# Optimization experiments

Hardware: AMD Instinct MI355X
Metric: run time of the kernel (lower is better)

The kernel has to match this reference:

```python
import jax, jax.numpy as jnp
import numpy as np

B, L, D = 2, 2048, 768
HID = 32           # saliency gate hidden dim
WINDOWS = (8, 32)  # sorted window sizes
CLAMP_MIN, CLAMP_MAX = 0.05, 0.95
SCALE = 1.0 / np.sqrt(D)  # memory_dim == d_model


def setup_inputs() -> dict:
    key = jax.random.key(0)
    ks = jax.random.split(key, 16)
    s = 0.02
    return {
        "hidden_states": jax.random.normal(ks[0], (B, L, D), jnp.float32),
        "saliency_scores": jax.random.uniform(ks[1], (B, L), jnp.float32),
        # SaliencyGate MLP: Linear(1->HID), SiLU, Linear(HID->D)
        "gw1": jax.random.normal(ks[2], (HID, 1), jnp.float32) * s,
        "gb1": jnp.zeros((HID,), jnp.float32),
        "gw2": jax.random.normal(ks[3], (D, HID), jnp.float32) * s,
        "gb2": jnp.zeros((D,), jnp.float32),
        # SelectiveMemory projections
        "wq": jax.random.normal(ks[4], (D, D), jnp.float32) * s,
        "bq": jnp.zeros((D,), jnp.float32),
        "wk": jax.random.normal(ks[5], (D, D), jnp.float32) * s,
        "bk": jnp.zeros((D,), jnp.float32),
        "wv": jax.random.normal(ks[6], (D, D), jnp.float32) * s,
        "bv": jnp.zeros((D,), jnp.float32),
        "wo": jax.random.normal(ks[7], (D, D), jnp.float32) * s,
        "bo": jnp.zeros((D,), jnp.float32),
    }


def _forward(hidden_states, saliency_scores, gw1, gb1, gw2, gb2,
             wq, bq, wk, bk, wv, bv, wo, bo):
    # ---- SaliencyGate: scalar score -> MLP -> sigmoid gate -> clamp ----
    s = saliency_scores[..., None]                          # (b, l, 1)
    h1 = jax.nn.silu(s @ gw1.T + gb1)                       # (b, l, HID)
    gates = jax.nn.sigmoid(h1 @ gw2.T + gb2)                # (b, l, D)
    gates = jnp.clip(gates, CLAMP_MIN, CLAMP_MAX)
    h = hidden_states * gates

    # ---- SelectiveMemory: multi-window local attention ----
    q = h @ wq.T + bq                                       # (b, l, D)
    k = h @ wk.T + bk
    v = h @ wv.T + bv
    # Torch pads hidden_states with zeros before k/v projection; linear of a
    # zero row equals the bias, so padded key/value rows are exactly bk / bv.
    contexts = []
    for w in WINDOWS:
        kp = jnp.concatenate(
            [jnp.broadcast_to(bk, (B, w - 1, D)), k], axis=1)  # (b, l+w-1, D)
        vp = jnp.concatenate(
            [jnp.broadcast_to(bv, (B, w - 1, D)), v], axis=1)
        idx = jnp.arange(L)[:, None] + jnp.arange(w)[None, :]  # (l, w)
        kw = kp[:, idx]                                        # (b, l, w, D)
        vw = vp[:, idx]
        scores = jnp.einsum('bld,blwd->blw', q, kw) * SCALE
        attn = jax.nn.softmax(scores, axis=-1)
        contexts.append(jnp.einsum('blw,blwd->bld', attn, vw))
    merged = (contexts[0] + contexts[1]) * 0.5 if len(contexts) > 1 else contexts[0]
    return h + merged @ wo.T + bo


def reference(hidden_states, saliency_scores, gw1, gb1, gw2, gb2,
              wq, bq, wk, bk, wv, bv, wo, bo):
    return _forward(hidden_states, saliency_scores, gw1, gb1, gw2, gb2,
                    wq, bq, wk, bk, wv, bv, wo, bo)
```

## Files before the change

### kernel.cpp

```cpp
#include <hip/hip_runtime.h>
#include <hip/hip_bf16.h>
#include <stdint.h>

#define Bb 2
#define Ll 2048
#define Dd 768
#define HID 32
#define BL (Bb*Ll)
#define KPAD 32
#define KROWS (KPAD+Ll+16)

typedef __hip_bfloat16 bf16;
typedef __attribute__((ext_vector_type(8))) short short8;
typedef __attribute__((ext_vector_type(4))) short short4s;
typedef __attribute__((ext_vector_type(4))) float floatx4;

__device__ __forceinline__ float b2f(short u) {
    union { float f; unsigned i; } x; x.i = ((unsigned)(unsigned short)u) << 16; return x.f;
}
__device__ __forceinline__ bf16 f2b(float x) { return __float2bfloat16(x); }
__device__ __forceinline__ short f2bs(float x) {
    bf16 t = __float2bfloat16(x);
    union { bf16 h; short s; } u; u.h = t; return u.s;
}

typedef __attribute__((address_space(1))) const unsigned int guint;
typedef __attribute__((address_space(3))) unsigned int luint;
__device__ __forceinline__ void gload16(const bf16* g, bf16* l) {
    __builtin_amdgcn_global_load_lds((guint*)g, (luint*)l, 16, 0, 0);
}

#define CONV_VB 2304
#define KP_VB   (Bb*48)
#define VT_VB   ((Bb*Dd*48)/256)
#define PREP_VB (CONV_VB+KP_VB+VT_VB)
#define GATE_VB (BL/8)
__global__ __launch_bounds__(256) void prep_gate_kernel(
        const float* __restrict__ wq, const float* __restrict__ wk,
        const float* __restrict__ wv, const float* __restrict__ wo,
        const float* __restrict__ bk, const float* __restrict__ bv,
        const float* __restrict__ hidden, const float* __restrict__ sal,
        const float* __restrict__ gw1, const float* __restrict__ gb1,
        const float* __restrict__ gw2, const float* __restrict__ gb2,
        bf16* __restrict__ wout, bf16* __restrict__ kp, bf16* __restrict__ vT,
        bf16* __restrict__ h_b) {
    __shared__ bf16 g2t[32 * 770];
    __shared__ float h1s[8][HID];
    int bx = blockIdx.x, tid = threadIdx.x;
    if (bx < CONV_VB) {
        int idx = bx * 256 + tid;
        const int per = Dd * Dd / 4;
        int w = idx / per, r = idx % per;
        const float* src = (w == 0) ? wq : (w == 1) ? wk : (w == 2) ? wv : wo;
        float4 v = reinterpret_cast<const float4*>(src)[r];
        bf16* o = wout + (size_t)w * Dd * Dd + (size_t)r * 4;
        o[0] = f2b(v.x); o[1] = f2b(v.y); o[2] = f2b(v.z); o[3] = f2b(v.w);
    } else if (bx < CONV_VB + KP_VB) {
        int pb = bx - CONV_VB;
        int b = pb / 48, c = pb % 48;
        int row = (c < 32) ? c : (KPAD + Ll + (c - 32));
        size_t base = ((size_t)b * KROWS + row) * Dd;
        for (int i = tid; i < Dd; i += 256)
            kp[base + i] = (c < 32) ? f2b(bk[i]) : f2b(0.f);
    } else if (bx < PREP_VB) {
        int o = (bx - CONV_VB - KP_VB) * 256 + tid;
        int b = o / (Dd * 48); int rem = o - b * Dd * 48;
        int n = rem / 48, c = rem % 48;
        int col = (c < 32) ? c : (KPAD + Ll + (c - 32));
        vT[((size_t)b * Dd + n) * KROWS + col] = (c < 32) ? f2b(bv[n]) : f2b(0.f);
    } else {
        int row0 = (bx - PREP_VB) * 8;
#pragma unroll
        for (int k2 = 0; k2 < 24; ++k2) {
            int o4 = tid + k2 * 256;
            float4 v = reinterpret_cast<const float4*>(gw2)[o4];
            int d = o4 >> 3, j = (o4 & 7) * 4;
            g2t[(j + 0) * 770 + d] = f2b(v.x);
            g2t[(j + 1) * 770 + d] = f2b(v.y);
            g2t[(j + 2) * 770 + d] = f2b(v.z);
            g2t[(j + 3) * 770 + d] = f2b(v.w);
        }
        {
            int rr = tid >> 5, j = tid & 31;
            float s = sal[row0 + rr];
            float x = s * gw1[j] + gb1[j];
            h1s[rr][j] = x / (1.f + __expf(-x));
        }
        __syncthreads();
#pragma unroll
        for (int dl = 0; dl < 3; ++dl) {
            int d = tid + dl * 256;
            float base = gb2[d];
            float acc[8];
#pragma unroll
            for (int rr = 0; rr < 8; ++rr) acc[rr] = base;
#pragma unroll
            for (int j = 0; j < HID; ++j) {
                float wj = b2f(*(const short*)&g2t[j * 770 + d]);
#pragma unroll
                for (int rr = 0; rr < 8; ++rr) acc[rr] += h1s[rr][j] * wj;
            }
#pragma unroll
            for (int rr = 0; rr < 8; ++rr) {
                float g = 1.f / (1.f + __expf(-acc[rr]));
                g = fminf(fmaxf(g, 0.05f), 0.95f);
                size_t off = (size_t)(row0 + rr) * Dd + d;
                h_b[off] = f2b(hidden[off] * g);
            }
        }
    }
}

template<int NF, int BK>
__device__ __forceinline__ void gemm_core(const bf16* __restrict__ Ag, const bf16* __restrict__ Wg,
                                          int m0, int n0, bf16* As, bf16* Bs,
                                          floatx4 (&acc)[4][NF]) {
    const int tid  = threadIdx.x;
    const int wave = tid >> 6, lane = tid & 63;
    const int lrow = lane & 15, koff = (lane >> 4) * 8;
    const int wm = (wave >> 1) * 64, wn = (wave & 1) * (NF * 16);
    const int RS = BK * 2;
    const char* Asb = (const char*)As;
    const char* Bsb = (const char*)Bs;

    for (int k0 = 0; k0 < Dd; k0 += BK) {
#pragma unroll
        for (int c = 0; c < BK / 16; ++c) {
            int p = tid * 16 + c * 4096;
            int r = p / RS;
            int o = (p % RS) ^ ((r & 7) << 4);
            gload16(Ag + (size_t)(m0 + r) * Dd + k0 + (o >> 1),
                    As + (wave * 1024 + c * 4096) / 2);
        }
#pragma unroll
        for (int c = 0; c < NF * BK / 64; ++c) {
            int p = tid * 16 + c * 4096;
            int r = p / RS;
            int o = (p % RS) ^ ((r & 7) << 4);
            gload16(Wg + (size_t)(n0 + r) * Dd + k0 + (o >> 1),
                    Bs + (wave * 1024 + c * 4096) / 2);
        }
        __syncthreads();
#pragma unroll
        for (int kk = 0; kk < BK; kk += 32) {
            short8 a[4], b[NF];
#pragma unroll
            for (int i = 0; i < 4; ++i) {
                int row = wm + i * 16 + lrow;
                int byt = row * RS + (((kk + koff) * 2) ^ ((row & 7) << 4));
                a[i] = *reinterpret_cast<const short8*>(Asb + byt);
            }
#pragma unroll
            for (int j = 0; j < NF; ++j) {
                int row = wn + j * 16 + lrow;
                int byt = row * RS + (((kk + koff) * 2) ^ ((row & 7) << 4));
                b[j] = *reinterpret_cast<const short8*>(Bsb + byt);
            }
#pragma unroll
            for (int i = 0; i < 4; ++i)
#pragma unroll
                for (int j = 0; j < NF; ++j)
                    acc[i][j] = __builtin_amdgcn_mfma_f32_16x16x32_bf16(a[i], b[j], acc[i][j], 0, 0, 0);
        }
        __syncthreads();
    }
}

__global__ __launch_bounds__(256, 2) void gemm_qkv(
        const bf16* __restrict__ A, const bf16* __restrict__ W3,
        const float* __restrict__ bq, const float* __restrict__ bk, const float* __restrict__ bv,
        bf16* __restrict__ qo, bf16* __restrict__ kp, bf16* __restrict__ vT) {
    __shared__ bf16 As[128 * 128];
    __shared__ bf16 Bs[128 * 128];
    int bid = blockIdx.x;
    int xcd = bid & 7, idx = bid >> 3;
    int mtile = (xcd >> 1) * 8 + (idx & 7);
    int ntile = (xcd & 1) * 9 + (idx >> 3);
    int tgt = ntile / 6;
    int n0 = (ntile % 6) * 128;
    int m0 = mtile * 128;
    const bf16* W = W3 + (size_t)tgt * Dd * Dd;
    const float* bias = (tgt == 0) ? bq : (tgt == 1) ? bk : bv;

    floatx4 acc[4][4] = {};
    gemm_core<4, 128>(A, W, m0, n0, As, Bs, acc);

    int wave = threadIdx.x >> 6, lane = threadIdx.x & 63;
    int wm = (wave >> 1) * 64, wn = (wave & 1) * 64;
    int crow = (lane >> 4) * 4, ccol = lane & 15;
#pragma unroll
    for (int i = 0; i < 4; ++i)
#pragma unroll
        for (int j = 0; j < 4; ++j) {
            int n = n0 + wn + j * 16 + ccol;
            float bb = bias[n];
            int m = m0 + wm + i * 16 + crow;
            int b_ = m >> 11, l = m & 2047;
            if (tgt == 2) {
                short4s pk;
#pragma unroll
                for (int rr = 0; rr < 4; ++rr) pk[rr] = f2bs(acc[i][j][rr] + bb);
                *reinterpret_cast<short4s*>(vT + ((size_t)b_ * Dd + n) * KROWS + KPAD + l) = pk;
            } else {
#pragma unroll
                for (int rr = 0; rr < 4; ++rr) {
                    size_t orow = (tgt == 0) ? (size_t)(m + rr)
                                             : ((size_t)b_ * KROWS + KPAD + l + rr);
                    bf16* outp = (tgt == 0) ? qo : kp;
                    outp[orow * Dd + n] = f2b(acc[i][j][rr] + bb);
                }
            }
        }
}

__global__ __launch_bounds__(256, 2) void gemm_out(
        const bf16* __restrict__ A, const bf16* __restrict__ W,
        const float* __restrict__ bias, const bf16* __restrict__ addend,
        float* __restrict__ out) {
    __shared__ bf16 As[128 * 64];
    __shared__ bf16 Bs[64 * 64];
    int bid = blockIdx.x;
    int xcd = bid & 7, idx = bid >> 3;
    int mtile = (xcd >> 1) * 8 + (idx & 7);
    int ntile = (xcd & 1) * 6 + (idx >> 3);
    int n0 = ntile * 64, m0 = mtile * 128;

    floatx4 acc[4][2] = {};
    gemm_core<2, 64>(A, W, m0, n0, As, Bs, acc);

    int wave = threadIdx.x >> 6, lane = threadIdx.x & 63;
    int wm = (wave >> 1) * 64, wn = (wave & 1) * 32;
    int crow = (lane >> 4) * 4, ccol = lane & 15;
#pragma unroll
    for (int i = 0; i < 4; ++i)
#pragma unroll
        for (int j = 0; j < 2; ++j) {
            int n = n0 + wn + j * 16 + ccol;
            float bb = bias[n];
#pragma unroll
            for (int rr = 0; rr < 4; ++rr) {
                int m = m0 + wm + i * 16 + crow + rr;
                size_t o = (size_t)m * Dd + n;
                out[o] = acc[i][j][rr] + bb + b2f(*(const short*)(addend + o));
            }
        }
}

__global__ __launch_bounds__(64) void attn_kernel(
        const bf16* __restrict__ q, const bf16* __restrict__ kp, const bf16* __restrict__ vT,
        bf16* __restrict__ merged) {
    __shared__ bf16 wlds[16 * 64];
    const int lane = threadIdx.x;
    const int bid = blockIdx.x;
    const int g = (bid & 7) * 32 + (bid >> 3);
    const int b = g >> 7, L0 = (g & 127) * 16;
    const int lrow = lane & 15, koff = (lane >> 4) * 8;
    const int crow = (lane >> 4) * 4, ccol = lane & 15;
    const float scale = 0.03608439182435161f;

    const bf16* qbase = q  + ((size_t)(b * Ll + L0 + lrow)) * Dd + koff;
    const bf16* kbase = kp + ((size_t)b * KROWS + L0 + lrow) * Dd + koff;
    floatx4 s[4] = {};
    for (int ks = 0; ks < 24; ++ks) {
        short8 a = *reinterpret_cast<const short8*>(qbase + ks * 32);
#pragma unroll
        for (int f = 0; f < 4; ++f) {
            short8 bb = *reinterpret_cast<const short8*>(kbase + (size_t)f * 16 * Dd + ks * 32);
            s[f] = __builtin_amdgcn_mfma_f32_16x16x32_bf16(a, bb, s[f], 0, 0, 0);
        }
    }
#pragma unroll
    for (int rr = 0; rr < 4; ++rr) {
        int r = crow + rr;
        float z[4], e[4];
#pragma unroll
        for (int f = 0; f < 4; ++f) {
            int j = f * 16 + ccol;
            bool valid = (j >= r + 1) && (j <= r + 32);
            z[f] = valid ? s[f][rr] * scale : -3.0e38f;
        }
        float m = fmaxf(fmaxf(z[0], z[1]), fmaxf(z[2], z[3]));
#pragma unroll
        for (int off = 1; off < 16; off <<= 1) m = fmaxf(m, __shfl_xor(m, off));
        float S32 = 0.f, S8 = 0.f;
#pragma unroll
        for (int f = 0; f < 4; ++f) {
            e[f] = __expf(z[f] - m);
            S32 += e[f];
            int j = f * 16 + ccol;
            S8 += ((j >= r + 25) && (j <= r + 32)) ? e[f] : 0.f;
        }
#pragma unroll
        for (int off = 1; off < 16; off <<= 1) {
            S32 += __shfl_xor(S32, off);
            S8  += __shfl_xor(S8, off);
        }
        float i32 = 0.5f / S32, i8 = 0.5f / S8;
#pragma unroll
        for (int f = 0; f < 4; ++f) {
            int j = f * 16 + ccol;
            float wgt = e[f] * i32 + (((j >= r + 25) && (j <= r + 32)) ? e[f] * i8 : 0.f);
            int byt = ((r * 64 + j) * 2) ^ ((r & 7) << 4);
            *reinterpret_cast<bf16*>(reinterpret_cast<char*>(wlds) + byt) = f2b(wgt);
        }
    }
    __syncthreads();

    short8 wa[2];
#pragma unroll
    for (int ks = 0; ks < 2; ++ks) {
        int byt = ((lrow * 64 + ks * 32 + koff) * 2) ^ ((lrow & 7) << 4);
        wa[ks] = *reinterpret_cast<const short8*>(reinterpret_cast<const char*>(wlds) + byt);
    }
    const bf16* vbase = vT + (size_t)b * Dd * KROWS + L0;
    bf16* obase = merged + ((size_t)(b * Ll + L0 + ccol)) * Dd;
    for (int c = 0; c < 6; ++c) {
#pragma unroll
        for (int fn = 0; fn < 8; ++fn) {
            int nr = c * 128 + fn * 16;
            floatx4 acc = {};
#pragma unroll
            for (int ks = 0; ks < 2; ++ks) {
                short8 bb = *reinterpret_cast<const short8*>(vbase + (size_t)(nr + lrow) * KROWS + ks * 32 + koff);
                acc = __builtin_amdgcn_mfma_f32_16x16x32_bf16(bb, wa[ks], acc, 0, 0, 0);
            }
            short4s pk;
#pragma unroll
            for (int rr = 0; rr < 4; ++rr) pk[rr] = f2bs(acc[rr]);
            *reinterpret_cast<short4s*>(obase + nr + crow) = pk;
        }
    }
}

extern "C" void kernel_launch(void* const* d_in, const int* in_sizes, int n_in,
                              void* d_out, int out_size, void* d_ws, size_t ws_size,
                              hipStream_t stream) {
    const float* hidden = (const float*)d_in[0];
    const float* sal    = (const float*)d_in[1];
    const float* gw1    = (const float*)d_in[2];
    const float* gb1    = (const float*)d_in[3];
    const float* gw2    = (const float*)d_in[4];
    const float* gb2    = (const float*)d_in[5];
    const float* wq     = (const float*)d_in[6];
    const float* bq     = (const float*)d_in[7];
    const float* wk     = (const float*)d_in[8];
    const float* bk     = (const float*)d_in[9];
    const float* wv     = (const float*)d_in[10];
    const float* bv     = (const float*)d_in[11];
    const float* wo     = (const float*)d_in[12];
    const float* bo     = (const float*)d_in[13];
    float* out = (float*)d_out;

    const size_t nBL  = (size_t)BL * Dd;
    const size_t nPad = (size_t)Bb * KROWS * Dd;
    char* p = (char*)d_ws;
    bf16* h_b = (bf16*)p; p += nBL * 2;
    bf16* q_b = (bf16*)p; p += nBL * 2;
    bf16* kpd = (bf16*)p; p += nPad * 2;
    bf16* vT  = (bf16*)p; p += nPad * 2;
    bf16* m_b = (bf16*)p; p += nBL * 2;
    bf16* w_b = (bf16*)p; p += (size_t)4 * Dd * Dd * 2;

    prep_gate_kernel<<<dim3(PREP_VB + GATE_VB), 256, 0, stream>>>(
        wq, wk, wv, wo, bk, bv, hidden, sal, gw1, gb1, gw2, gb2, w_b, kpd, vT, h_b);
    gemm_qkv<<<dim3(576), 256, 0, stream>>>(h_b, w_b, bq, bk, bv, q_b, kpd, vT);
    attn_kernel<<<dim3(256), 64, 0, stream>>>(q_b, kpd, vT, m_b);
    gemm_out<<<dim3(384), 256, 0, stream>>>(m_b, w_b + (size_t)3 * Dd * Dd, bo, h_b, out);
}
```

Baseline: 79.68 us.

## Split attention kernel across 8 waves with split-K scores and LDS reduction

```diff
diff --git a/kernel.cpp b/kernel.cpp
--- a/kernel.cpp
+++ b/kernel.cpp
@@ -246,11 +246,14 @@
         }
 }
 
-__global__ __launch_bounds__(64) void attn_kernel(
+#define AW 8
+__global__ __launch_bounds__(512) void attn_kernel(
         const bf16* __restrict__ q, const bf16* __restrict__ kp, const bf16* __restrict__ vT,
         bf16* __restrict__ merged) {
-    __shared__ bf16 wlds[16 * 64];
-    const int lane = threadIdx.x;
+    __shared__ float Sp[AW][16][66];
+    __shared__ bf16 wlds[AW][16 * 64];
+    const int tid = threadIdx.x;
+    const int wv = tid >> 6, lane = tid & 63;
     const int bid = blockIdx.x;
     const int g = (bid & 7) * 32 + (bid >> 3);
     const int b = g >> 7, L0 = (g & 127) * 16;
@@ -258,17 +261,25 @@
     const int crow = (lane >> 4) * 4, ccol = lane & 15;
     const float scale = 0.03608439182435161f;
 
-    const bf16* qbase = q  + ((size_t)(b * Ll + L0 + lrow)) * Dd + koff;
-    const bf16* kbase = kp + ((size_t)b * KROWS + L0 + lrow) * Dd + koff;
-    floatx4 s[4] = {};
-    for (int ks = 0; ks < 24; ++ks) {
+    const bf16* qbase = q  + ((size_t)(b * Ll + L0 + lrow)) * Dd + koff + wv * 96;
+    const bf16* kbase = kp + ((size_t)b * KROWS + L0 + lrow) * Dd + koff + wv * 96;
+    floatx4 s4[4] = {};
+#pragma unroll
+    for (int ks = 0; ks < 3; ++ks) {
         short8 a = *reinterpret_cast<const short8*>(qbase + ks * 32);
 #pragma unroll
         for (int f = 0; f < 4; ++f) {
             short8 bb = *reinterpret_cast<const short8*>(kbase + (size_t)f * 16 * Dd + ks * 32);
-            s[f] = __builtin_amdgcn_mfma_f32_16x16x32_bf16(a, bb, s[f], 0, 0, 0);
-        }
-    }
+            s4[f] = __builtin_amdgcn_mfma_f32_16x16x32_bf16(a, bb, s4[f], 0, 0, 0);
+        }
+    }
+#pragma unroll
+    for (int f = 0; f < 4; ++f)
+#pragma unroll
+        for (int rr = 0; rr < 4; ++rr)
+            Sp[wv][crow + rr][f * 16 + ccol] = s4[f][rr];
+    __syncthreads();
+
 #pragma unroll
     for (int rr = 0; rr < 4; ++rr) {
         int r = crow + rr;
@@ -276,8 +287,11 @@
 #pragma unroll
         for (int f = 0; f < 4; ++f) {
             int j = f * 16 + ccol;
+            float v = 0.f;
+#pragma unroll
+            for (int w = 0; w < AW; ++w) v += Sp[w][r][j];
             bool valid = (j >= r + 1) && (j <= r + 32);
-            z[f] = valid ? s[f][rr] * scale : -3.0e38f;
+            z[f] = valid ? v * scale : -3.0e38f;
         }
         float m = fmaxf(fmaxf(z[0], z[1]), fmaxf(z[2], z[3]));
 #pragma unroll
@@ -301,34 +315,31 @@
             int j = f * 16 + ccol;
             float wgt = e[f] * i32 + (((j >= r + 25) && (j <= r + 32)) ? e[f] * i8 : 0.f);
             int byt = ((r * 64 + j) * 2) ^ ((r & 7) << 4);
-            *reinterpret_cast<bf16*>(reinterpret_cast<char*>(wlds) + byt) = f2b(wgt);
-        }
-    }
-    __syncthreads();
+            *reinterpret_cast<bf16*>(reinterpret_cast<char*>(wlds[wv]) + byt) = f2b(wgt);
+        }
+    }
 
     short8 wa[2];
 #pragma unroll
     for (int ks = 0; ks < 2; ++ks) {
         int byt = ((lrow * 64 + ks * 32 + koff) * 2) ^ ((lrow & 7) << 4);
-        wa[ks] = *reinterpret_cast<const short8*>(reinterpret_cast<const char*>(wlds) + byt);
+        wa[ks] = *reinterpret_cast<const short8*>(reinterpret_cast<const char*>(wlds[wv]) + byt);
     }
     const bf16* vbase = vT + (size_t)b * Dd * KROWS + L0;
     bf16* obase = merged + ((size_t)(b * Ll + L0 + ccol)) * Dd;
-    for (int c = 0; c < 6; ++c) {
-#pragma unroll
-        for (int fn = 0; fn < 8; ++fn) {
-            int nr = c * 128 + fn * 16;
-            floatx4 acc = {};
-#pragma unroll
-            for (int ks = 0; ks < 2; ++ks) {
-                short8 bb = *reinterpret_cast<const short8*>(vbase + (size_t)(nr + lrow) * KROWS + ks * 32 + koff);
-                acc = __builtin_amdgcn_mfma_f32_16x16x32_bf16(bb, wa[ks], acc, 0, 0, 0);
-            }
-            short4s pk;
-#pragma unroll
-            for (int rr = 0; rr < 4; ++rr) pk[rr] = f2bs(acc[rr]);
-            *reinterpret_cast<short4s*>(obase + nr + crow) = pk;
-        }
+#pragma unroll
+    for (int fn = 0; fn < 6; ++fn) {
+        int nr = wv * 96 + fn * 16;
+        floatx4 acc = {};
+#pragma unroll
+        for (int ks = 0; ks < 2; ++ks) {
+            short8 bb = *reinterpret_cast<const short8*>(vbase + (size_t)(nr + lrow) * KROWS + ks * 32 + koff);
+            acc = __builtin_amdgcn_mfma_f32_16x16x32_bf16(bb, wa[ks], acc, 0, 0, 0);
+        }
+        short4s pk;
+#pragma unroll
+        for (int rr = 0; rr < 4; ++rr) pk[rr] = f2bs(acc[rr]);
+        *reinterpret_cast<short4s*>(obase + nr + crow) = pk;
     }
 }
 
@@ -364,6 +375,6 @@
     prep_gate_kernel<<<dim3(PREP_VB + GATE_VB), 256, 0, stream>>>(
         wq, wk, wv, wo, bk, bv, hidden, sal, gw1, gb1, gw2, gb2, w_b, kpd, vT, h_b);
     gemm_qkv<<<dim3(576), 256, 0, stream>>>(h_b, w_b, bq, bk, bv, q_b, kpd, vT);
-    attn_kernel<<<dim3(256), 64, 0, stream>>>(q_b, kpd, vT, m_b);
+    attn_kernel<<<dim3(256), 512, 0, stream>>>(q_b, kpd, vT, m_b);
     gemm_out<<<dim3(384), 256, 0, stream>>>(m_b, w_b + (size_t)3 * Dd * Dd, bo, h_b, out);
 }
```

Measured after the change: 76.86 us. 1.04x faster.
